# Optimization experiments

Measured on AMD Instinct MI355X. Metric: run time of the kernel, lower is better.

## Reference

```python
import jax, jax.numpy as jnp
import numpy as np
import math

IN_DIM = 4096
OUT_DIM = 4096
BLOCK_SIZE = 64
RECT_NUM = 128
DEPTH = 3
PADDED_DIM = 4096  # 2**ceil(log2(in_dim)); in_dim is already a power of 2 -> pad = 0
NUM_BLOCK_GROUPS = PADDED_DIM // BLOCK_SIZE  # 64
BLOCK_WIDTH = PADDED_DIM // RECT_NUM         # 32
BLOCK_HEIGHT = OUT_DIM // RECT_NUM           # 32


def fwht(x):
    """Fast Walsh-Hadamard transform along last dim. x: [B, D], D power of 2."""
    B, D = x.shape
    h = 1
    while h < D:  # static loop, log2(D) iterations
        x = x.reshape(B, D // (2 * h), 2, h)
        a = x[:, :, 0, :]
        b = x[:, :, 1, :]
        x = jnp.stack([a + b, a - b], axis=2).reshape(B, D)
        h *= 2
    return x


def setup_inputs() -> dict:
    key = jax.random.key(0)
    k1, k2, k3 = jax.random.split(key, 3)
    x = jax.random.normal(k1, (4, 4096, IN_DIM), dtype=jnp.float32)
    # inner_B: (depth-1) block-diagonal stages, stacked: [depth-1, num_block_groups, bs, bs]
    inner_B = jax.random.normal(k2, (DEPTH - 1, NUM_BLOCK_GROUPS, BLOCK_SIZE, BLOCK_SIZE), dtype=jnp.float32)
    final_B = 0.1 * jax.random.normal(k3, (RECT_NUM, BLOCK_WIDTH, BLOCK_HEIGHT), dtype=jnp.float32)
    return {"x": x, "inner_B": inner_B, "final_B": final_B}


def reference(x, inner_B, final_B):
    orig_shape = x.shape
    xf = x.reshape(-1, IN_DIM)  # pad == 0, so padded view == flattened view
    B = xf.shape[0]
    scale = 1.0 / math.sqrt(PADDED_DIM)
    for i in range(inner_B.shape[0]):  # static loop over depth-1 butterfly stages
        xb = xf.reshape(B, NUM_BLOCK_GROUPS, BLOCK_SIZE)
        xb = jnp.einsum('bni,nio->bno', xb, inner_B[i])
        xf = fwht(xb.reshape(B, PADDED_DIM)) * scale
    xr = xf.reshape(B, RECT_NUM, BLOCK_WIDTH)
    out = jnp.einsum('bni,nio->bno', xr, final_B)
    return out.reshape(*orig_shape[:-1], OUT_DIM)
```

## Files before the change

kernel.cpp:

```cpp
#include <hip/hip_runtime.h>
#include <hip/hip_bf16.h>


typedef __attribute__((ext_vector_type(8))) short bf16x8;
typedef __attribute__((ext_vector_type(4))) short bf16x4;
typedef __attribute__((ext_vector_type(4))) float f32x4;

#define MFMA16(a, b, c) __builtin_amdgcn_mfma_f32_16x16x32_bf16((a), (b), (c), 0, 0, 0)

__device__ __forceinline__ short f2bf(float f) {
    unsigned int u; __builtin_memcpy(&u, &f, 4);
    u += 0x7FFFu + ((u >> 16) & 1u);
    return (short)(u >> 16);
}
__device__ __forceinline__ int swz(int b, int d) {
    int key = (b + (d >> 8)) & 15;
    return (b << 12) | (d & 0xFC0) | ((((d >> 2) & 15) ^ key) << 2) | (d & 3);
}

__global__ void prep_inner(const float* __restrict__ B, short* __restrict__ out) {
    int e = blockIdx.x * 256 + threadIdx.x;
    int jj = e & 7, lane = (e >> 3) & 63, fid = e >> 9;
    int ks = fid & 1, it = (fid >> 1) & 3, g = (fid >> 3) & 63, l = fid >> 9;
    int j  = ks * 32 + ((lane >> 4) << 3) + jj;
    int op = it * 16 + (lane & 15);
    const float* Bg = B + (((l * 64 + g) * 64 + j) * 64);
    float acc = 0.f;
    #pragma unroll
    for (int k = 0; k < 64; ++k) {
        float f = Bg[k];
        acc += (__builtin_popcount(k & op) & 1) ? -f : f;
    }
    out[e] = f2bf(acc * 0.015625f);
}

__global__ void prep_final(const float* __restrict__ F, short* __restrict__ out) {
    int e = blockIdx.x * 256 + threadIdx.x;
    int ww = e & 7, lane = (e >> 3) & 63, fid = e >> 9;
    int ot = fid & 1, r = fid >> 1;
    int w = ((lane >> 4) << 3) + ww;
    int o = ot * 16 + (lane & 15);
    out[e] = f2bf(F[(r * 32 + w) * 32 + o]);
}

__global__ __launch_bounds__(512) void bh_main(
        const float* __restrict__ Xg,
        const short* __restrict__ CW,
        const short* __restrict__ FW,
        float* __restrict__ Og) {
    __shared__ short sm[16 * 4096];
    const int tid  = threadIdx.x;
    const int lane = tid & 63;
    const int wave = tid >> 6;
    const long row0 = (long)blockIdx.x * 16;

    bf16x8 Hf[2][4];
    {
        int n0 = lane & 15, mb = (lane >> 4) << 3;
        #pragma unroll
        for (int ks = 0; ks < 2; ++ks)
            #pragma unroll
            for (int nt = 0; nt < 4; ++nt) {
                bf16x8 h;
                #pragma unroll
                for (int jj = 0; jj < 8; ++jj) {
                    int m = ks * 32 + mb + jj, n = nt * 16 + n0;
                    h[jj] = (short)((__builtin_popcount(m & n) & 1) ? 0xBF80 : 0x3F80);
                }
                Hf[ks][nt] = h;
            }
    }

    {
        const float* src = Xg + row0 * 4096;
        const int d = tid * 8;
        #pragma unroll
        for (int b = 0; b < 16; ++b) {
            f32x4 v0 = *(const f32x4*)(src + (long)b * 4096 + d);
            f32x4 v1 = *(const f32x4*)(src + (long)b * 4096 + d + 4);
            bf16x4 q0 = { f2bf(v0[0]), f2bf(v0[1]), f2bf(v0[2]), f2bf(v0[3]) };
            bf16x4 q1 = { f2bf(v1[0]), f2bf(v1[1]), f2bf(v1[2]), f2bf(v1[3]) };
            *(bf16x4*)(sm + swz(b, d))     = q0;
            *(bf16x4*)(sm + swz(b, d + 4)) = q1;
        }
    }
    __syncthreads();

    #pragma unroll 1
    for (int l = 0; l < 2; ++l) {
        {
            const int b = lane & 15;
            const int koff = (lane >> 4) << 3;
            const short* Wl = CW + l * 262144;
            #pragma unroll 2
            for (int gi = 0; gi < 8; ++gi) {
                int g = wave * 8 + gi;
                bf16x8 wf[4][2];
                #pragma unroll
                for (int it = 0; it < 4; ++it)
                    #pragma unroll
                    for (int ks = 0; ks < 2; ++ks)
                        wf[it][ks] = *(const bf16x8*)(Wl + ((g * 8 + it * 2 + ks) * 64 + lane) * 8);
                bf16x8 xf[2];
                #pragma unroll
                for (int ks = 0; ks < 2; ++ks) {
                    int d = g * 64 + ks * 32 + koff;
                    bf16x4 a0 = *(const bf16x4*)(sm + swz(b, d));
                    bf16x4 a1 = *(const bf16x4*)(sm + swz(b, d + 4));
                    xf[ks] = bf16x8{a0[0],a0[1],a0[2],a0[3],a1[0],a1[1],a1[2],a1[3]};
                }
                #pragma unroll
                for (int it = 0; it < 4; ++it) {
                    f32x4 acc = {0.f, 0.f, 0.f, 0.f};
                    acc = MFMA16(wf[it][0], xf[0], acc);
                    acc = MFMA16(wf[it][1], xf[1], acc);
                    int i0 = it * 16 + ((lane >> 4) << 2);
                    bf16x4 o4 = { f2bf(acc[0]), f2bf(acc[1]), f2bf(acc[2]), f2bf(acc[3]) };
                    *(bf16x4*)(sm + swz(b, g * 64 + i0)) = o4;
                }
            }
        }
        __syncthreads();

        {
            const int ba = lane & 15;
            const int moff = (lane >> 4) << 3;
            #pragma unroll 1
            for (int s = 0; s < 2; ++s) {
                const int i0 = (wave * 2 + s) << 2;
                bf16x4 rd[2][8];
                #pragma unroll
                for (int ks = 0; ks < 2; ++ks)
                    #pragma unroll
                    for (int mm = 0; mm < 8; ++mm)
                        rd[ks][mm] = *(const bf16x4*)(sm + swz(ba, (ks * 32 + moff + mm) * 64 + i0));
                f32x4 acc[4][4];
                #pragma unroll
                for (int c = 0; c < 4; ++c) {
                    bf16x8 af0, af1;
                    #pragma unroll
                    for (int mm = 0; mm < 8; ++mm) { af0[mm] = rd[0][mm][c]; af1[mm] = rd[1][mm][c]; }
                    #pragma unroll
                    for (int nt = 0; nt < 4; ++nt) {
                        f32x4 a = {0.f, 0.f, 0.f, 0.f};
                        a = MFMA16(af0, Hf[0][nt], a);
                        a = MFMA16(af1, Hf[1][nt], a);
                        acc[c][nt] = a;
                    }
                }
                const int n0 = lane & 15;
                const int bq = (lane >> 4) << 2;
                #pragma unroll
                for (int nt = 0; nt < 4; ++nt) {
                    int n = nt * 16 + n0;
                    #pragma unroll
                    for (int q = 0; q < 4; ++q) {
                        int b = bq + q;
                        bf16x4 o4 = { f2bf(acc[0][nt][q]), f2bf(acc[1][nt][q]),
                                      f2bf(acc[2][nt][q]), f2bf(acc[3][nt][q]) };
                        *(bf16x4*)(sm + swz(b, n * 64 + i0)) = o4;
                    }
                }
            }
        }
        __syncthreads();
    }

    {
        const int b = lane & 15;
        const int woff = (lane >> 4) << 3;
        float* Orow = Og + (row0 + b) * 4096;
        #pragma unroll 2
        for (int ri = 0; ri < 16; ++ri) {
            int r = wave * 16 + ri;
            bf16x8 wf0 = *(const bf16x8*)(FW + ((r * 2 + 0) * 64 + lane) * 8);
            bf16x8 wf1 = *(const bf16x8*)(FW + ((r * 2 + 1) * 64 + lane) * 8);
            int d = r * 32 + woff;
            bf16x4 a0 = *(const bf16x4*)(sm + swz(b, d));
            bf16x4 a1 = *(const bf16x4*)(sm + swz(b, d + 4));
            bf16x8 xf = {a0[0],a0[1],a0[2],a0[3],a1[0],a1[1],a1[2],a1[3]};
            #pragma unroll
            for (int ot = 0; ot < 2; ++ot) {
                f32x4 acc = {0.f, 0.f, 0.f, 0.f};
                acc = MFMA16(ot ? wf1 : wf0, xf, acc);
                int o0 = ot * 16 + ((lane >> 4) << 2);
                *(f32x4*)(Orow + r * 32 + o0) = acc;
            }
        }
    }
}

extern "C" void kernel_launch(void* const* d_in, const int* in_sizes, int n_in,
                              void* d_out, int out_size, void* d_ws, size_t ws_size,
                              hipStream_t stream) {
    const float* x  = (const float*)d_in[0];
    const float* iB = (const float*)d_in[1];
    const float* fB = (const float*)d_in[2];
    short* CW = (short*)d_ws;
    short* FW = CW + 524288;

    prep_inner<<<2048, 256, 0, stream>>>(iB, CW);
    prep_final<<<512, 256, 0, stream>>>(fB, FW);
    bh_main<<<1024, 512, 0, stream>>>(x, CW, FW, (float*)d_out);
}
```

Before: 533.3 us.

## Double threads per block in main kernel and use shuffle-based FWHT in weight prep

The main kernel now launches 1024 threads (16 waves) per block instead of 512, halving each wave's share of groups, rows, and output tiles in every stage so more waves can hide LDS and MFMA latency. The inner-weight prep kernel drops its per-element 64-term popcount loop and instead loads one weight row per wave and applies the Hadamard with xor shuffles, scattering results into the MFMA fragment layout. The prep rewrite cuts redundant arithmetic and global reads. The larger block raises per-CU thread count while LDS use per block is unchanged, so occupancy is limited by LDS and registers under the new launch bounds.

```diff
diff --git a/kernel.cpp b/kernel.cpp
--- a/kernel.cpp
+++ b/kernel.cpp
@@ -18,20 +18,22 @@
     return (b << 12) | (d & 0xFC0) | ((((d >> 2) & 15) ^ key) << 2) | (d & 3);
 }
 
-__global__ void prep_inner(const float* __restrict__ B, short* __restrict__ out) {
-    int e = blockIdx.x * 256 + threadIdx.x;
-    int jj = e & 7, lane = (e >> 3) & 63, fid = e >> 9;
-    int ks = fid & 1, it = (fid >> 1) & 3, g = (fid >> 3) & 63, l = fid >> 9;
-    int j  = ks * 32 + ((lane >> 4) << 3) + jj;
-    int op = it * 16 + (lane & 15);
-    const float* Bg = B + (((l * 64 + g) * 64 + j) * 64);
-    float acc = 0.f;
+__global__ __launch_bounds__(256) void prep_inner(const float* __restrict__ B, short* __restrict__ out) {
+    int rid  = blockIdx.x * 4 + (threadIdx.x >> 6);
+    int lane = threadIdx.x & 63;
+    float v = B[rid * 64 + lane];
     #pragma unroll
-    for (int k = 0; k < 64; ++k) {
-        float f = Bg[k];
-        acc += (__builtin_popcount(k & op) & 1) ? -f : f;
-    }
-    out[e] = f2bf(acc * 0.015625f);
+    for (int m = 1; m < 64; m <<= 1) {
+        float p = __shfl_xor(v, m, 64);
+        v = (lane & m) ? (p - v) : (v + p);
+    }
+    int l = rid >> 12, g = (rid >> 6) & 63, j = rid & 63;
+    int o = lane;
+    int jj = j & 7, lhi = (j >> 3) & 3, ks = j >> 5;
+    int it = o >> 4;
+    int lane_dst = lhi * 16 + (o & 15);
+    int fid = l * 512 + g * 8 + it * 2 + ks;
+    out[(fid * 64 + lane_dst) * 8 + jj] = f2bf(v * 0.015625f);
 }
 
 __global__ void prep_final(const float* __restrict__ F, short* __restrict__ out) {
@@ -43,7 +45,7 @@
     out[e] = f2bf(F[(r * 32 + w) * 32 + o]);
 }
 
-__global__ __launch_bounds__(512) void bh_main(
+__global__ __launch_bounds__(1024, 4) void bh_main(
         const float* __restrict__ Xg,
         const short* __restrict__ CW,
         const short* __restrict__ FW,
@@ -73,9 +75,11 @@
 
     {
         const float* src = Xg + row0 * 4096;
-        const int d = tid * 8;
+        const int d   = (tid & 511) * 8;
+        const int bb0 = (tid >> 9) * 8;
         #pragma unroll
-        for (int b = 0; b < 16; ++b) {
+        for (int bb = 0; bb < 8; ++bb) {
+            int b = bb0 + bb;
             f32x4 v0 = *(const f32x4*)(src + (long)b * 4096 + d);
             f32x4 v1 = *(const f32x4*)(src + (long)b * 4096 + d + 4);
             bf16x4 q0 = { f2bf(v0[0]), f2bf(v0[1]), f2bf(v0[2]), f2bf(v0[3]) };
@@ -93,8 +97,8 @@
             const int koff = (lane >> 4) << 3;
             const short* Wl = CW + l * 262144;
             #pragma unroll 2
-            for (int gi = 0; gi < 8; ++gi) {
-                int g = wave * 8 + gi;
+            for (int gi = 0; gi < 4; ++gi) {
+                int g = wave * 4 + gi;
                 bf16x8 wf[4][2];
                 #pragma unroll
                 for (int it = 0; it < 4; ++it)
@@ -125,41 +129,38 @@
         {
             const int ba = lane & 15;
             const int moff = (lane >> 4) << 3;
-            #pragma unroll 1
-            for (int s = 0; s < 2; ++s) {
-                const int i0 = (wave * 2 + s) << 2;
-                bf16x4 rd[2][8];
-                #pragma unroll
-                for (int ks = 0; ks < 2; ++ks)
-                    #pragma unroll
-                    for (int mm = 0; mm < 8; ++mm)
-                        rd[ks][mm] = *(const bf16x4*)(sm + swz(ba, (ks * 32 + moff + mm) * 64 + i0));
-                f32x4 acc[4][4];
-                #pragma unroll
-                for (int c = 0; c < 4; ++c) {
-                    bf16x8 af0, af1;
-                    #pragma unroll
-                    for (int mm = 0; mm < 8; ++mm) { af0[mm] = rd[0][mm][c]; af1[mm] = rd[1][mm][c]; }
-                    #pragma unroll
-                    for (int nt = 0; nt < 4; ++nt) {
-                        f32x4 a = {0.f, 0.f, 0.f, 0.f};
-                        a = MFMA16(af0, Hf[0][nt], a);
-                        a = MFMA16(af1, Hf[1][nt], a);
-                        acc[c][nt] = a;
-                    }
-                }
-                const int n0 = lane & 15;
-                const int bq = (lane >> 4) << 2;
+            const int i0 = wave << 2;
+            bf16x4 rd[2][8];
+            #pragma unroll
+            for (int ks = 0; ks < 2; ++ks)
+                #pragma unroll
+                for (int mm = 0; mm < 8; ++mm)
+                    rd[ks][mm] = *(const bf16x4*)(sm + swz(ba, (ks * 32 + moff + mm) * 64 + i0));
+            f32x4 acc[4][4];
+            #pragma unroll
+            for (int c = 0; c < 4; ++c) {
+                bf16x8 af0, af1;
+                #pragma unroll
+                for (int mm = 0; mm < 8; ++mm) { af0[mm] = rd[0][mm][c]; af1[mm] = rd[1][mm][c]; }
                 #pragma unroll
                 for (int nt = 0; nt < 4; ++nt) {
-                    int n = nt * 16 + n0;
-                    #pragma unroll
-                    for (int q = 0; q < 4; ++q) {
-                        int b = bq + q;
-                        bf16x4 o4 = { f2bf(acc[0][nt][q]), f2bf(acc[1][nt][q]),
-                                      f2bf(acc[2][nt][q]), f2bf(acc[3][nt][q]) };
-                        *(bf16x4*)(sm + swz(b, n * 64 + i0)) = o4;
-                    }
+                    f32x4 a = {0.f, 0.f, 0.f, 0.f};
+                    a = MFMA16(af0, Hf[0][nt], a);
+                    a = MFMA16(af1, Hf[1][nt], a);
+                    acc[c][nt] = a;
+                }
+            }
+            const int n0 = lane & 15;
+            const int bq = (lane >> 4) << 2;
+            #pragma unroll
+            for (int nt = 0; nt < 4; ++nt) {
+                int n = nt * 16 + n0;
+                #pragma unroll
+                for (int q = 0; q < 4; ++q) {
+                    int b = bq + q;
+                    bf16x4 o4 = { f2bf(acc[0][nt][q]), f2bf(acc[1][nt][q]),
+                                  f2bf(acc[2][nt][q]), f2bf(acc[3][nt][q]) };
+                    *(bf16x4*)(sm + swz(b, n * 64 + i0)) = o4;
                 }
             }
         }
@@ -171,8 +172,8 @@
         const int woff = (lane >> 4) << 3;
         float* Orow = Og + (row0 + b) * 4096;
         #pragma unroll 2
-        for (int ri = 0; ri < 16; ++ri) {
-            int r = wave * 16 + ri;
+        for (int ri = 0; ri < 8; ++ri) {
+            int r = wave * 8 + ri;
             bf16x8 wf0 = *(const bf16x8*)(FW + ((r * 2 + 0) * 64 + lane) * 8);
             bf16x8 wf1 = *(const bf16x8*)(FW + ((r * 2 + 1) * 64 + lane) * 8);
             int d = r * 32 + woff;
@@ -201,5 +202,5 @@
 
     prep_inner<<<2048, 256, 0, stream>>>(iB, CW);
     prep_final<<<512, 256, 0, stream>>>(fB, FW);
-    bh_main<<<1024, 512, 0, stream>>>(x, CW, FW, (float*)d_out);
-}
+    bh_main<<<1024, 1024, 0, stream>>>(x, CW, FW, (float*)d_out);
+}
```

Result: slower. 588.8 us (+10.4%).
